# Performance work log

Measured on AMD Instinct MI355X. Metric: run time of the kernel, lower is better.

The kernel has to match this reference:

```python
import jax, jax.numpy as jnp
import numpy as np

B, S, D, H = 2, 2048, 1024, 16
DK = D // H
ROPE_BASE = 10000


def _rope_tables(seq_len, dim):
    # RotaryEmbedding.__call__: freqs [S, dim/2], emb = concat([freqs, freqs]) -> [S, dim]
    inv_freq = 1.0 / (ROPE_BASE ** (jnp.arange(0, dim, 2, dtype=jnp.float32) / dim))
    t = jnp.arange(seq_len, dtype=jnp.float32)
    freqs = jnp.outer(t, inv_freq)
    emb = jnp.concatenate([freqs, freqs], axis=-1)
    return jnp.cos(emb), jnp.sin(emb)


def _apply_rope(x, cos, sin):
    # Faithful to apply_rotary_pos_emb: interleaved even/odd channel rotation
    cos = cos[None, None, :, :]  # [1,1,S,DK]
    sin = sin[None, None, :, :]
    x1 = x[..., 0::2]
    x2 = x[..., 1::2]
    r1 = x1 * cos[..., 0::2] - x2 * sin[..., 1::2]
    r2 = x1 * sin[..., 0::2] + x2 * cos[..., 1::2]
    return jnp.stack([r1, r2], axis=-1).reshape(x.shape)


def setup_inputs() -> dict:
    key = jax.random.key(0)
    ks = jax.random.split(key, 11)
    xavier = lambda k: jax.random.uniform(k, (D, D), jnp.float32,
                                          -jnp.sqrt(6.0 / (D + D)), jnp.sqrt(6.0 / (D + D)))
    return {
        "query": jax.random.normal(ks[0], (B, S, D), jnp.float32),
        "key": jax.random.normal(ks[1], (B, S, D), jnp.float32),
        "value": jax.random.normal(ks[2], (B, S, D), jnp.float32),
        "Wq": xavier(ks[3]), "bq": jnp.zeros((D,), jnp.float32),
        "Wk": xavier(ks[4]), "bk": jnp.zeros((D,), jnp.float32),
        "Wv": xavier(ks[5]), "bv": jnp.zeros((D,), jnp.float32),
        "Wo": xavier(ks[6]), "bo": jnp.zeros((D,), jnp.float32),
    }


def reference(query, key, value, Wq, bq, Wk, bk, Wv, bv, Wo, bo):
    def split_heads(x):  # [B,S,D] -> [B,H,S,DK]
        return x.reshape(B, S, H, DK).transpose(0, 2, 1, 3)

    q = split_heads(query @ Wq + bq)
    k = split_heads(key @ Wk + bk)
    v = split_heads(value @ Wv + bv)

    cos, sin = _rope_tables(S, DK)
    q = _apply_rope(q, cos, sin)
    k = _apply_rope(k, cos, sin)

    scores = jnp.einsum("bhqd,bhkd->bhqk", q, k) / jnp.sqrt(jnp.float32(DK))
    causal = jnp.tril(jnp.ones((S, S), dtype=bool))
    scores = jnp.where(causal, scores, jnp.float32(-1e10))
    attn = jax.nn.softmax(scores, axis=-1)
    out = jnp.einsum("bhqk,bhkd->bhqd", attn, v)  # [B,H,S,DK]
    out = out.transpose(0, 2, 1, 3).reshape(B, S, D)
    return out @ Wo + bo
```

## Files before the change

### kernel.cpp

```cpp
#include <hip/hip_runtime.h>
#include <hip/hip_bf16.h>
#include <math.h>

#define B_ 2
#define S_ 2048
#define D_ 1024
#define H_ 16
#define DK_ 64

#define ROPE_C 0.4152410118609203f
#define LOG2E 1.4426950408889634f

typedef float f4 __attribute__((ext_vector_type(4)));
typedef short s8 __attribute__((ext_vector_type(8)));

__device__ __forceinline__ ushort f2b(float f) {
  union { float f; uint u; } v; v.f = f;
  uint u = v.u + 0x7fffu + ((v.u >> 16) & 1u);
  return (ushort)(u >> 16);
}

__device__ __forceinline__ float b2f(ushort u) {
  union { uint u; float f; } v; v.u = ((uint)u) << 16;
  return v.f;
}

__device__ __forceinline__ void async16(const ushort* g, ushort* l) {
  __builtin_amdgcn_global_load_lds(
      (const __attribute__((address_space(1))) uint*)g,
      (__attribute__((address_space(3))) uint*)l, 16, 0, 0);
}

__global__ __launch_bounds__(256) void conv_x(const float* __restrict__ in,
                                              ushort* __restrict__ out) {
  int idx = (blockIdx.x * 256 + threadIdx.x) * 8;
  float4 a = *(const float4*)&in[idx];
  float4 b = *(const float4*)&in[idx + 4];
  ushort tmp[8] = {f2b(a.x), f2b(a.y), f2b(a.z), f2b(a.w),
                   f2b(b.x), f2b(b.y), f2b(b.z), f2b(b.w)};
  *(uint4*)&out[idx] = *(uint4*)tmp;
}

__global__ __launch_bounds__(256) void transpose_w(const float* __restrict__ W,
                                                   ushort* __restrict__ Wt) {
  __shared__ ushort T[64][65];
  const int t = threadIdx.x;
  const int k0 = blockIdx.x * 64, n0 = blockIdx.y * 64;
  #pragma unroll
  for (int i = 0; i < 16; ++i) {
    int e = t + i * 256, r = e >> 6, c = e & 63;
    T[c][r] = f2b(W[(size_t)(k0 + r) * D_ + n0 + c]);
  }
  __syncthreads();
  #pragma unroll
  for (int i = 0; i < 16; ++i) {
    int e = t + i * 256, r = e >> 6, c = e & 63;
    Wt[(size_t)(n0 + r) * D_ + k0 + c] = T[r][c];
  }
}

template <int MODE>
__global__ __launch_bounds__(256) void gemm_mfma(
    const ushort* __restrict__ A0, const ushort* __restrict__ A1,
    const ushort* __restrict__ A2, const ushort* __restrict__ Bt,
    const float* __restrict__ bb0, const float* __restrict__ bb1,
    const float* __restrict__ bb2,
    ushort* __restrict__ oq, ushort* __restrict__ ok, ushort* __restrict__ ov,
    float* __restrict__ oo) {
  __shared__ ushort As[128 * 32];
  __shared__ ushort Bs[128 * 32];
  __shared__ ushort Es[(MODE == 0) ? 9216 : 1];

  const int t = threadIdx.x, w = t >> 6, l = t & 63;
  const int m0 = blockIdx.x * 128, n0 = blockIdx.y * 128;
  const int wm = (w >> 1) * 64, wn = (w & 1) * 64;
  const int lm = l & 15, h8 = (l >> 4) * 8, q4 = (l >> 4) * 4;
  const int hb = l >> 4;

  const ushort* A;
  const float* bias;
  int mat = 0;
  if constexpr (MODE == 0) {
    mat = n0 >> 10;
    A = (mat == 0) ? A0 : (mat == 1) ? A1 : A2;
    bias = (mat == 0) ? bb0 : (mat == 1) ? bb1 : bb2;
  } else {
    A = A0; bias = bb0;
  }

  const int srow = w * 32 + (l >> 2);
  const int pb = l & 3;
  const int lb = pb ^ (srow & 3);
  const ushort* gA = A + (size_t)(m0 + srow) * D_ + lb * 8;
  const ushort* gB = Bt + (size_t)(n0 + srow) * D_ + lb * 8;
  ushort* lA = As + w * 1024;
  ushort* lB = Bs + w * 1024;

  f4 acc[4][4];
  #pragma unroll
  for (int i = 0; i < 4; ++i)
    #pragma unroll
    for (int j = 0; j < 4; ++j) acc[i][j] = (f4){0.f, 0.f, 0.f, 0.f};

  for (int k0 = 0; k0 < D_; k0 += 32) {
    async16(gA + k0, lA);
    async16(gA + 16 * D_ + k0, lA + 512);
    async16(gB + k0, lB);
    async16(gB + 16 * D_ + k0, lB + 512);
    __syncthreads();
    s8 af[4], bfr[4];
    #pragma unroll
    for (int mt = 0; mt < 4; ++mt) {
      int ra = wm + mt * 16 + lm;
      af[mt] = *(const s8*)&As[ra * 32 + ((hb ^ (ra & 3)) << 3)];
    }
    #pragma unroll
    for (int nt = 0; nt < 4; ++nt) {
      int rb = wn + nt * 16 + lm;
      bfr[nt] = *(const s8*)&Bs[rb * 32 + ((hb ^ (rb & 3)) << 3)];
    }
    #pragma unroll
    for (int mt = 0; mt < 4; ++mt)
      #pragma unroll
      for (int nt = 0; nt < 4; ++nt)
        acc[mt][nt] = __builtin_amdgcn_mfma_f32_16x16x32_bf16(af[mt], bfr[nt], acc[mt][nt], 0, 0, 0);
    __syncthreads();
  }

  if constexpr (MODE == 2) {
    #pragma unroll
    for (int nt = 0; nt < 4; ++nt) {
      int n = n0 + wn + nt * 16 + lm;
      float bv = bias[n];
      #pragma unroll
      for (int mt = 0; mt < 4; ++mt)
        #pragma unroll
        for (int r = 0; r < 4; ++r)
          oo[(size_t)(m0 + wm + mt * 16 + q4 + r) * D_ + n] = acc[mt][nt][r] + bv;
    }
  } else {
    ushort* dst = (mat == 0) ? oq : (mat == 1) ? ok : ov;
    const int nm0 = n0 & 1023;
    #pragma unroll
    for (int p = 0; p < 2; ++p) {
      if ((w >> 1) == p) {
        #pragma unroll
        for (int nt = 0; nt < 4; ++nt) {
          int col = wn + nt * 16 + lm;
          float bv = bias[nm0 + col];
          #pragma unroll
          for (int mt = 0; mt < 4; ++mt)
            #pragma unroll
            for (int r = 0; r < 4; ++r)
              Es[(mt * 16 + q4 + r) * 144 + col] = f2b(acc[mt][nt][r] + bv);
        }
      }
      __syncthreads();
      #pragma unroll
      for (int i = 0; i < 4; ++i) {
        int e = t + i * 256, row = e >> 4, ch = e & 15;
        *(uint4*)&dst[(size_t)(m0 + p * 64 + row) * D_ + nm0 + ch * 8] =
            *(const uint4*)&Es[row * 144 + ch * 8];
      }
      __syncthreads();
    }
  }
}

__global__ __launch_bounds__(256) void rope_pass(
    const ushort* __restrict__ qtmp, const ushort* __restrict__ ktmp,
    const ushort* __restrict__ vtmp,
    ushort* __restrict__ qfb, ushort* __restrict__ kfb,
    ushort* __restrict__ vtb) {
  __shared__ ushort T[64][72];
  const int t = threadIdx.x;
  const int bh = blockIdx.x, st = blockIdx.y;
  const int b = bh >> 4, h = bh & 15;
  const int s0 = st * 64;
  const int r = t >> 2, c0 = (t & 3) * 16;
  const int s = s0 + r;

  float cs[16], sn[16];
  const float pos = (float)s;
  #pragma unroll
  for (int j = 0; j < 16; ++j) {
    float invf = exp2f(-(float)((c0 + j) & 31) * ROPE_C);
    __sincosf(pos * invf, &sn[j], &cs[j]);
  }

  const size_t src = ((size_t)(b * S_ + s)) * D_ + h * 64 + c0;
  const size_t dstqk = ((size_t)bh * S_ + s) * DK_ + c0;

  #pragma unroll
  for (int tensor = 0; tensor < 2; ++tensor) {
    const ushort* in = tensor ? ktmp : qtmp;
    ushort* out = tensor ? kfb : qfb;
    const float scale = tensor ? 1.f : 0.18033688011112042f;
    uint4 raw0 = *(const uint4*)&in[src];
    uint4 raw1 = *(const uint4*)&in[src + 8];
    ushort xr[16];
    *(uint4*)&xr[0] = raw0;
    *(uint4*)&xr[8] = raw1;
    float x[16];
    #pragma unroll
    for (int j = 0; j < 16; ++j) x[j] = b2f(xr[j]);
    ushort o[16];
    #pragma unroll
    for (int j = 0; j < 16; j += 2) {
      float e = x[j] * cs[j] - x[j + 1] * sn[j + 1];
      float d = x[j] * sn[j] + x[j + 1] * cs[j + 1];
      o[j] = f2b(e * scale);
      o[j + 1] = f2b(d * scale);
    }
    *(uint4*)&out[dstqk] = *(const uint4*)&o[0];
    *(uint4*)&out[dstqk + 8] = *(const uint4*)&o[8];
  }

  {
    uint4 raw0 = *(const uint4*)&vtmp[src];
    uint4 raw1 = *(const uint4*)&vtmp[src + 8];
    ushort xr[16];
    *(uint4*)&xr[0] = raw0;
    *(uint4*)&xr[8] = raw1;
    #pragma unroll
    for (int j = 0; j < 16; ++j) T[c0 + j][r] = xr[j];
    __syncthreads();
    const size_t dstv = ((size_t)bh * DK_ + r) * S_ + s0 + c0;
    *(uint4*)&vtb[dstv] = *(const uint4*)&T[r][c0];
    *(uint4*)&vtb[dstv + 8] = *(const uint4*)&T[r][c0 + 8];
  }
}

__global__ __launch_bounds__(256, 3) void attn_mfma(const ushort* __restrict__ qf,
                                                    const ushort* __restrict__ kf,
                                                    const ushort* __restrict__ vtf,
                                                    ushort* __restrict__ ctx) {
  __shared__ ushort Ks[2][4096];
  __shared__ ushort Vs[2][4096];
  __shared__ ushort Ps[64][72];

  const int t = threadIdx.x, w = t >> 6, l = t & 63;
  const int bh = blockIdx.x, qt = 31 - (int)blockIdx.y;
  const int i0 = qt * 64;
  const int lm = l & 15, hb = l >> 4, h8 = hb * 8, q4 = hb * 4, w16 = w * 16;
  const size_t base = (size_t)bh * S_ * DK_;
  const int b = bh >> 4, h = bh & 15;

  const int sr = l >> 3, pbk = l & 7;
  const int rA = w * 16 + sr, rB = rA + 8;
  const int swS = (pbk ^ sr) << 3;
  const ushort* gkA = kf + base + (size_t)rA * DK_ + swS;
  const ushort* gkB = kf + base + (size_t)rB * DK_ + swS;
  const ushort* gvA = vtf + base + (size_t)rA * S_ + swS;
  const ushort* gvB = vtf + base + (size_t)rB * S_ + swS;

#define STAGE(bf, j0)                                       \
  {                                                         \
    ushort* lk = &Ks[bf][w * 1024];                         \
    ushort* lv = &Vs[bf][w * 1024];                         \
    async16(gkA + (size_t)(j0) * DK_, lk);                  \
    async16(gkB + (size_t)(j0) * DK_, lk + 512);            \
    async16(gvA + (j0), lv);                                \
    async16(gvB + (j0), lv + 512);                          \
  }

  const ushort* qp = qf + base + (size_t)(i0 + w16 + lm) * DK_ + h8;
  const s8 bq0 = *(const s8*)qp;
  const s8 bq1 = *(const s8*)(qp + 32);

  const int swr = lm & 7;
  const int cA = (hb ^ swr) << 3;
  const int cB = ((hb + 4) ^ swr) << 3;

  STAGE(0, 0);

  f4 O[4];
  #pragma unroll
  for (int i = 0; i < 4; ++i) O[i] = (f4){0.f, 0.f, 0.f, 0.f};
  float m_ = -1e30f, l_ = 0.f;

  __syncthreads();

  for (int jt = 0; jt <= qt; ++jt) {
    const int cur = jt & 1;
    if (jt < qt) STAGE(cur ^ 1, (jt + 1) * 64);
    const ushort* Kb = Ks[cur];
    const ushort* Vb = Vs[cur];

    f4 st[4];
    __builtin_amdgcn_s_setprio(1);
    #pragma unroll
    for (int nt = 0; nt < 4; ++nt) {
      const ushort* kRow = Kb + (nt * 16 + lm) * 64;
      s8 a0 = *(const s8*)&kRow[cA];
      s8 a1 = *(const s8*)&kRow[cB];
      f4 a = (f4){0.f, 0.f, 0.f, 0.f};
      a = __builtin_amdgcn_mfma_f32_16x16x32_bf16(a0, bq0, a, 0, 0, 0);
      a = __builtin_amdgcn_mfma_f32_16x16x32_bf16(a1, bq1, a, 0, 0, 0);
      st[nt] = a;
    }
    __builtin_amdgcn_s_setprio(0);

    if (jt == qt) {
      #pragma unroll
      for (int nt = 0; nt < 4; ++nt)
        #pragma unroll
        for (int r = 0; r < 4; ++r)
          if (nt * 16 + q4 + r > w16 + lm) st[nt][r] = -1e30f;
    }

    float x0 = fmaxf(fmaxf(st[0][0], st[0][1]), fmaxf(st[0][2], st[0][3]));
    float x1 = fmaxf(fmaxf(st[1][0], st[1][1]), fmaxf(st[1][2], st[1][3]));
    float x2 = fmaxf(fmaxf(st[2][0], st[2][1]), fmaxf(st[2][2], st[2][3]));
    float x3 = fmaxf(fmaxf(st[3][0], st[3][1]), fmaxf(st[3][2], st[3][3]));
    float pm = fmaxf(fmaxf(x0, x1), fmaxf(x2, x3));
    pm = fmaxf(pm, __shfl_xor(pm, 16));
    pm = fmaxf(pm, __shfl_xor(pm, 32));

    const bool stable = __all(pm <= m_ + 4.0f);
    float mn = m_, alpha = 1.f;
    if (!stable) {
      mn = fmaxf(m_, pm);
      alpha = exp2f(m_ - mn);
      m_ = mn;
    }

    #pragma unroll
    for (int nt = 0; nt < 4; ++nt)
      #pragma unroll
      for (int r = 0; r < 4; ++r)
        st[nt][r] = exp2f(st[nt][r] - mn);
    float s0 = (st[0][0] + st[0][1]) + (st[0][2] + st[0][3]);
    float s1 = (st[1][0] + st[1][1]) + (st[1][2] + st[1][3]);
    float s2 = (st[2][0] + st[2][1]) + (st[2][2] + st[2][3]);
    float s3 = (st[3][0] + st[3][1]) + (st[3][2] + st[3][3]);
    float ps = (s0 + s1) + (s2 + s3);
    ps += __shfl_xor(ps, 16);
    ps += __shfl_xor(ps, 32);

    if (stable) {
      l_ += ps;
    } else {
      l_ = l_ * alpha + ps;
      float ar[4];
      #pragma unroll
      for (int r = 0; r < 4; ++r) ar[r] = __shfl(alpha, q4 + r);
      #pragma unroll
      for (int nt = 0; nt < 4; ++nt)
        #pragma unroll
        for (int r = 0; r < 4; ++r) O[nt][r] *= ar[r];
    }

    #pragma unroll
    for (int nt = 0; nt < 4; ++nt) {
      ushort pk[4] = {f2b(st[nt][0]), f2b(st[nt][1]), f2b(st[nt][2]), f2b(st[nt][3])};
      *(uint2*)&Ps[w16 + lm][nt * 16 + q4] = *(const uint2*)pk;
    }
    s8 ap0 = *(const s8*)&Ps[w16 + lm][h8];
    s8 ap1 = *(const s8*)&Ps[w16 + lm][h8 + 32];

    __builtin_amdgcn_s_setprio(1);
    #pragma unroll
    for (int nt = 0; nt < 4; ++nt) {
      const ushort* vRow = Vb + (nt * 16 + lm) * 64;
      s8 v0 = *(const s8*)&vRow[cA];
      s8 v1 = *(const s8*)&vRow[cB];
      O[nt] = __builtin_amdgcn_mfma_f32_16x16x32_bf16(ap0, v0, O[nt], 0, 0, 0);
      O[nt] = __builtin_amdgcn_mfma_f32_16x16x32_bf16(ap1, v1, O[nt], 0, 0, 0);
    }
    __builtin_amdgcn_s_setprio(0);

    __syncthreads();
  }

  float il[4];
  #pragma unroll
  for (int r = 0; r < 4; ++r) il[r] = 1.f / __shfl(l_, q4 + r);
  #pragma unroll
  for (int nt = 0; nt < 4; ++nt)
    #pragma unroll
    for (int r = 0; r < 4; ++r)
      Ps[w16 + q4 + r][nt * 16 + lm] = f2b(O[nt][r] * il[r]);
  __syncthreads();
  #pragma unroll
  for (int i = 0; i < 2; ++i) {
    int e = t + i * 256, row = e >> 3, ch = e & 7;
    int s = i0 + row;
    *(uint4*)&ctx[((size_t)(b * S_ + s)) * D_ + h * 64 + ch * 8] =
        *(const uint4*)&Ps[row][ch * 8];
  }
#undef STAGE
}

extern "C" void kernel_launch(void* const* d_in, const int* in_sizes, int n_in,
                              void* d_out, int out_size, void* d_ws, size_t ws_size,
                              hipStream_t stream) {
  const float* q_in = (const float*)d_in[0];
  const float* k_in = (const float*)d_in[1];
  const float* v_in = (const float*)d_in[2];
  const float* Wq = (const float*)d_in[3];
  const float* bq = (const float*)d_in[4];
  const float* Wk = (const float*)d_in[5];
  const float* bk = (const float*)d_in[6];
  const float* Wv = (const float*)d_in[7];
  const float* bv = (const float*)d_in[8];
  const float* Wo = (const float*)d_in[9];
  const float* bo = (const float*)d_in[10];

  const size_t NE = (size_t)B_ * S_ * D_;
  ushort* Xbq = (ushort*)d_ws;
  ushort* Xbk = Xbq + NE;
  ushort* Xbv = Xbk + NE;
  ushort* Wtqkv = Xbv + NE;
  ushort* Wto = Wtqkv + 3 * 1024 * 1024;
  ushort* qtmp = Wto + 1024 * 1024;
  ushort* ktmp = qtmp + NE;
  ushort* vtmp = ktmp + NE;
  ushort* qfb = vtmp + NE;
  ushort* kfb = qfb + NE;
  ushort* vtb = kfb + NE;
  ushort* ctxb = qtmp;

  conv_x<<<2048, 256, 0, stream>>>(q_in, Xbq);
  conv_x<<<2048, 256, 0, stream>>>(k_in, Xbk);
  conv_x<<<2048, 256, 0, stream>>>(v_in, Xbv);
  transpose_w<<<dim3(16, 16), 256, 0, stream>>>(Wq, Wtqkv);
  transpose_w<<<dim3(16, 16), 256, 0, stream>>>(Wk, Wtqkv + 1024 * 1024);
  transpose_w<<<dim3(16, 16), 256, 0, stream>>>(Wv, Wtqkv + 2 * 1024 * 1024);
  transpose_w<<<dim3(16, 16), 256, 0, stream>>>(Wo, Wto);

  gemm_mfma<0><<<dim3(32, 24), 256, 0, stream>>>(
      Xbq, Xbk, Xbv, Wtqkv, bq, bk, bv, qtmp, ktmp, vtmp, nullptr);

  rope_pass<<<dim3(32, 32), 256, 0, stream>>>(qtmp, ktmp, vtmp, qfb, kfb, vtb);

  attn_mfma<<<dim3(32, 32), 256, 0, stream>>>(qfb, kfb, vtb, ctxb);

  gemm_mfma<2><<<dim3(32, 8), 256, 0, stream>>>(
      ctxb, ctxb, ctxb, Wto, bo, bo, bo, nullptr, nullptr, nullptr,
      (float*)d_out);
}
```

Measured before the change: 257.7 us.

## Merge prep kernels, double-buffer GEMM LDS, swizzle attention P buffer, raise occupancy

Fuses the three activation-conversion launches and four weight-transpose launches into a single prep kernel, cutting launch overhead. The GEMM now double-buffers its LDS tiles, prefetching the next K slice while MFMAs run, and raises wave priority around the MFMA block; the epilogue scratch shares the same LDS array. The attention kernel replaces its padded P buffer with an XOR-swizzled 64x64 layout, packs to bf16 with v_cvt_pk_bf16_f32, and raises the occupancy hint from 3 to 4 blocks per CU. The risks are extra register pressure at the higher occupancy target and round-to-nearest differences from the hardware pack instruction.

```diff
diff --git a/kernel.cpp b/kernel.cpp
--- a/kernel.cpp
+++ b/kernel.cpp
@@ -25,37 +25,54 @@
   return v.f;
 }
 
+__device__ __forceinline__ uint cvtpk(float a, float b) {
+  uint r;
+  asm("v_cvt_pk_bf16_f32 %0, %1, %2" : "=v"(r) : "v"(a), "v"(b));
+  return r;
+}
+
 __device__ __forceinline__ void async16(const ushort* g, ushort* l) {
   __builtin_amdgcn_global_load_lds(
       (const __attribute__((address_space(1))) uint*)g,
       (__attribute__((address_space(3))) uint*)l, 16, 0, 0);
 }
 
-__global__ __launch_bounds__(256) void conv_x(const float* __restrict__ in,
-                                              ushort* __restrict__ out) {
-  int idx = (blockIdx.x * 256 + threadIdx.x) * 8;
-  float4 a = *(const float4*)&in[idx];
-  float4 b = *(const float4*)&in[idx + 4];
-  ushort tmp[8] = {f2b(a.x), f2b(a.y), f2b(a.z), f2b(a.w),
-                   f2b(b.x), f2b(b.y), f2b(b.z), f2b(b.w)};
-  *(uint4*)&out[idx] = *(uint4*)tmp;
-}
-
-__global__ __launch_bounds__(256) void transpose_w(const float* __restrict__ W,
-                                                   ushort* __restrict__ Wt) {
+__global__ __launch_bounds__(256) void prep_all(
+    const float* __restrict__ q_in, const float* __restrict__ k_in,
+    const float* __restrict__ v_in,
+    ushort* __restrict__ Xbq, ushort* __restrict__ Xbk, ushort* __restrict__ Xbv,
+    const float* __restrict__ Wq, const float* __restrict__ Wk,
+    const float* __restrict__ Wv, const float* __restrict__ Wo,
+    ushort* __restrict__ Wtqkv, ushort* __restrict__ Wto) {
   __shared__ ushort T[64][65];
-  const int t = threadIdx.x;
-  const int k0 = blockIdx.x * 64, n0 = blockIdx.y * 64;
-  #pragma unroll
-  for (int i = 0; i < 16; ++i) {
-    int e = t + i * 256, r = e >> 6, c = e & 63;
-    T[c][r] = f2b(W[(size_t)(k0 + r) * D_ + n0 + c]);
-  }
-  __syncthreads();
-  #pragma unroll
-  for (int i = 0; i < 16; ++i) {
-    int e = t + i * 256, r = e >> 6, c = e & 63;
-    Wt[(size_t)(n0 + r) * D_ + k0 + c] = T[r][c];
+  const int bid = blockIdx.x, t = threadIdx.x;
+  if (bid < 6144) {
+    const int m = bid >> 11;
+    const float* in = (m == 0) ? q_in : (m == 1) ? k_in : v_in;
+    ushort* out = (m == 0) ? Xbq : (m == 1) ? Xbk : Xbv;
+    int idx = ((bid & 2047) * 256 + t) * 8;
+    float4 a = *(const float4*)&in[idx];
+    float4 b = *(const float4*)&in[idx + 4];
+    ushort tmp[8] = {f2b(a.x), f2b(a.y), f2b(a.z), f2b(a.w),
+                     f2b(b.x), f2b(b.y), f2b(b.z), f2b(b.w)};
+    *(uint4*)&out[idx] = *(uint4*)tmp;
+  } else {
+    const int tb = bid - 6144;
+    const int m = tb >> 8;
+    const float* W = (m == 0) ? Wq : (m == 1) ? Wk : (m == 2) ? Wv : Wo;
+    ushort* Wt = (m == 3) ? Wto : Wtqkv + (size_t)m * 1024 * 1024;
+    const int k0 = (tb & 15) * 64, n0 = ((tb >> 4) & 15) * 64;
+    #pragma unroll
+    for (int i = 0; i < 16; ++i) {
+      int e = t + i * 256, r = e >> 6, c = e & 63;
+      T[c][r] = f2b(W[(size_t)(k0 + r) * D_ + n0 + c]);
+    }
+    __syncthreads();
+    #pragma unroll
+    for (int i = 0; i < 16; ++i) {
+      int e = t + i * 256, r = e >> 6, c = e & 63;
+      Wt[(size_t)(n0 + r) * D_ + k0 + c] = T[r][c];
+    }
   }
 }
 
@@ -67,14 +84,13 @@
     const float* __restrict__ bb2,
     ushort* __restrict__ oq, ushort* __restrict__ ok, ushort* __restrict__ ov,
     float* __restrict__ oo) {
-  __shared__ ushort As[128 * 32];
-  __shared__ ushort Bs[128 * 32];
-  __shared__ ushort Es[(MODE == 0) ? 9216 : 1];
+  __shared__ ushort SM[16384];
+  ushort* Es = SM;
 
   const int t = threadIdx.x, w = t >> 6, l = t & 63;
   const int m0 = blockIdx.x * 128, n0 = blockIdx.y * 128;
   const int wm = (w >> 1) * 64, wn = (w & 1) * 64;
-  const int lm = l & 15, h8 = (l >> 4) * 8, q4 = (l >> 4) * 4;
+  const int lm = l & 15, q4 = (l >> 4) * 4;
   const int hb = l >> 4;
 
   const ushort* A;
@@ -93,8 +109,16 @@
   const int lb = pb ^ (srow & 3);
   const ushort* gA = A + (size_t)(m0 + srow) * D_ + lb * 8;
   const ushort* gB = Bt + (size_t)(n0 + srow) * D_ + lb * 8;
-  ushort* lA = As + w * 1024;
-  ushort* lB = Bs + w * 1024;
+
+#define GSTAGE(bf, kk)                                   \
+  {                                                      \
+    ushort* lA = SM + (bf) * 4096 + w * 1024;            \
+    ushort* lB = SM + 8192 + (bf) * 4096 + w * 1024;     \
+    async16(gA + (kk), lA);                              \
+    async16(gA + 16 * D_ + (kk), lA + 512);              \
+    async16(gB + (kk), lB);                              \
+    async16(gB + 16 * D_ + (kk), lB + 512);              \
+  }
 
   f4 acc[4][4];
   #pragma unroll
@@ -102,28 +126,32 @@
     #pragma unroll
     for (int j = 0; j < 4; ++j) acc[i][j] = (f4){0.f, 0.f, 0.f, 0.f};
 
+  GSTAGE(0, 0);
+  __syncthreads();
+
   for (int k0 = 0; k0 < D_; k0 += 32) {
-    async16(gA + k0, lA);
-    async16(gA + 16 * D_ + k0, lA + 512);
-    async16(gB + k0, lB);
-    async16(gB + 16 * D_ + k0, lB + 512);
-    __syncthreads();
+    const int bf = (k0 >> 5) & 1;
+    if (k0 + 32 < D_) GSTAGE(bf ^ 1, k0 + 32);
+    const ushort* Asb = SM + bf * 4096;
+    const ushort* Bsb = SM + 8192 + bf * 4096;
     s8 af[4], bfr[4];
     #pragma unroll
     for (int mt = 0; mt < 4; ++mt) {
       int ra = wm + mt * 16 + lm;
-      af[mt] = *(const s8*)&As[ra * 32 + ((hb ^ (ra & 3)) << 3)];
+      af[mt] = *(const s8*)&Asb[ra * 32 + ((hb ^ (ra & 3)) << 3)];
     }
     #pragma unroll
     for (int nt = 0; nt < 4; ++nt) {
       int rb = wn + nt * 16 + lm;
-      bfr[nt] = *(const s8*)&Bs[rb * 32 + ((hb ^ (rb & 3)) << 3)];
-    }
+      bfr[nt] = *(const s8*)&Bsb[rb * 32 + ((hb ^ (rb & 3)) << 3)];
+    }
+    __builtin_amdgcn_s_setprio(1);
     #pragma unroll
     for (int mt = 0; mt < 4; ++mt)
       #pragma unroll
       for (int nt = 0; nt < 4; ++nt)
         acc[mt][nt] = __builtin_amdgcn_mfma_f32_16x16x32_bf16(af[mt], bfr[nt], acc[mt][nt], 0, 0, 0);
+    __builtin_amdgcn_s_setprio(0);
     __syncthreads();
   }
 
@@ -165,6 +193,7 @@
       __syncthreads();
     }
   }
+#undef GSTAGE
 }
 
 __global__ __launch_bounds__(256) void rope_pass(
@@ -231,13 +260,13 @@
   }
 }
 
-__global__ __launch_bounds__(256, 3) void attn_mfma(const ushort* __restrict__ qf,
+__global__ __launch_bounds__(256, 4) void attn_mfma(const ushort* __restrict__ qf,
                                                     const ushort* __restrict__ kf,
                                                     const ushort* __restrict__ vtf,
                                                     ushort* __restrict__ ctx) {
   __shared__ ushort Ks[2][4096];
   __shared__ ushort Vs[2][4096];
-  __shared__ ushort Ps[64][72];
+  __shared__ ushort PsS[4096];
 
   const int t = threadIdx.x, w = t >> 6, l = t & 63;
   const int bh = blockIdx.x, qt = 31 - (int)blockIdx.y;
@@ -271,6 +300,8 @@
   const int swr = lm & 7;
   const int cA = (hb ^ swr) << 3;
   const int cB = ((hb + 4) ^ swr) << 3;
+  const int prow = (w16 + lm) * 64;
+  const int psub = ((hb & 1) << 2) + ((hb >> 1) ^ swr);
 
   STAGE(0, 0);
 
@@ -353,11 +384,14 @@
 
     #pragma unroll
     for (int nt = 0; nt < 4; ++nt) {
-      ushort pk[4] = {f2b(st[nt][0]), f2b(st[nt][1]), f2b(st[nt][2]), f2b(st[nt][3])};
-      *(uint2*)&Ps[w16 + lm][nt * 16 + q4] = *(const uint2*)pk;
-    }
-    s8 ap0 = *(const s8*)&Ps[w16 + lm][h8];
-    s8 ap1 = *(const s8*)&Ps[w16 + lm][h8 + 32];
+      uint2 pp;
+      pp.x = cvtpk(st[nt][0], st[nt][1]);
+      pp.y = cvtpk(st[nt][2], st[nt][3]);
+      const int pidx = prow + ((((nt << 1) + (hb >> 1)) ^ swr) << 3) + ((hb & 1) << 2);
+      *(uint2*)&PsS[pidx] = pp;
+    }
+    s8 ap0 = *(const s8*)&PsS[prow + cA];
+    s8 ap1 = *(const s8*)&PsS[prow + cB];
 
     __builtin_amdgcn_s_setprio(1);
     #pragma unroll
@@ -379,15 +413,18 @@
   #pragma unroll
   for (int nt = 0; nt < 4; ++nt)
     #pragma unroll
-    for (int r = 0; r < 4; ++r)
-      Ps[w16 + q4 + r][nt * 16 + lm] = f2b(O[nt][r] * il[r]);
+    for (int r = 0; r < 4; ++r) {
+      int row = w16 + q4 + r, col = nt * 16 + lm;
+      PsS[row * 64 + ((((col >> 3) ^ (row & 7)) << 3)) + (col & 7)] =
+          f2b(O[nt][r] * il[r]);
+    }
   __syncthreads();
   #pragma unroll
   for (int i = 0; i < 2; ++i) {
     int e = t + i * 256, row = e >> 3, ch = e & 7;
     int s = i0 + row;
     *(uint4*)&ctx[((size_t)(b * S_ + s)) * D_ + h * 64 + ch * 8] =
-        *(const uint4*)&Ps[row][ch * 8];
+        *(const uint4*)&PsS[row * 64 + ((ch ^ (row & 7)) << 3)];
   }
 #undef STAGE
 }
@@ -421,13 +458,8 @@
   ushort* vtb = kfb + NE;
   ushort* ctxb = qtmp;
 
-  conv_x<<<2048, 256, 0, stream>>>(q_in, Xbq);
-  conv_x<<<2048, 256, 0, stream>>>(k_in, Xbk);
-  conv_x<<<2048, 256, 0, stream>>>(v_in, Xbv);
-  transpose_w<<<dim3(16, 16), 256, 0, stream>>>(Wq, Wtqkv);
-  transpose_w<<<dim3(16, 16), 256, 0, stream>>>(Wk, Wtqkv + 1024 * 1024);
-  transpose_w<<<dim3(16, 16), 256, 0, stream>>>(Wv, Wtqkv + 2 * 1024 * 1024);
-  transpose_w<<<dim3(16, 16), 256, 0, stream>>>(Wo, Wto);
+  prep_all<<<7168, 256, 0, stream>>>(q_in, k_in, v_in, Xbq, Xbk, Xbv,
+                                     Wq, Wk, Wv, Wo, Wtqkv, Wto);
 
   gemm_mfma<0><<<dim3(32, 24), 256, 0, stream>>>(
       Xbq, Xbk, Xbv, Wtqkv, bq, bk, bv, qtmp, ktmp, vtmp, nullptr);
```

Measured after the change: 228.7 us. -11.2%, faster.
